# Optimization experiments

Measured on AMD Instinct MI355X. Metric: run time of the kernel, lower is better.

## Reference

```python
import jax, jax.numpy as jnp
import numpy as np

BETA = 0.9
THRESHOLD = 1.0
ATAN_ALPHA = 2.0  # snntorch ATan surrogate default


def setup_inputs() -> dict:
    key = jax.random.key(0)
    k1, k2 = jax.random.split(key)
    T, B, NI, NO = 100, 128, 2048, 1024
    x = jax.random.normal(k1, (T, B, NI), dtype=jnp.float32)
    # Kaiming-uniform-ish init like nn.Linear
    bound = 1.0 / np.sqrt(NI)
    W = jax.random.uniform(k2, (NO, NI), dtype=jnp.float32, minval=-bound, maxval=bound)
    return {"x": x, "W": W}


def _heaviside(u):
    return (u > 0).astype(u.dtype)


def reference(x, W):
    # cur[t] = x[t] @ W.T for all timesteps at once: [T, B, NO]
    cur = jnp.einsum('tbi,oi->tbo', x, W)

    def step(mem, cur_t):
        # snntorch Leaky (reset_mechanism='subtract'):
        #   reset = heaviside(mem_prev - threshold)   (detached)
        #   mem   = beta * mem_prev + cur - reset * threshold
        #   spk   = heaviside(mem - threshold)
        reset = _heaviside(mem - THRESHOLD)
        mem_new = BETA * mem + cur_t - reset * THRESHOLD
        spk = _heaviside(mem_new - THRESHOLD)
        return mem_new, (spk, mem_new)

    mem0 = jnp.zeros(cur.shape[1:], dtype=cur.dtype)  # [B, NO]
    _, (spk_rec, mem_rec) = jax.lax.scan(step, mem0, cur)
    return spk_rec, mem_rec
```

## Files before the change

### kernel.cpp

```cpp
#include <hip/hip_runtime.h>

#define T_STEPS 100
#define BATCH   128
#define NI      2048
#define NO      1024
#define M_TOT   (T_STEPS * BATCH)
#define TOTAL   (T_STEPS * BATCH * NO)
#define BNTOT   (BATCH * NO)
#define X_ELEMS (M_TOT * NI)

#define BMf 128
#define BNf 128
#define BKf 32
#define LDT 132
#define NXB (NO / BNf)
#define NYB (M_TOT/BMf)

__global__ __launch_bounds__(256, 2) void gemm_chain512(const float* __restrict__ X,
                                                        const float* __restrict__ W,
                                                        float* __restrict__ p0,
                                                        float* __restrict__ p1,
                                                        float* __restrict__ p2,
                                                        float* __restrict__ p3) {
    __shared__ float As[BKf][LDT];
    __shared__ float Bs[BKf][LDT];

    const int orig  = blockIdx.x;
    const int xcd   = orig & 7;
    const int q     = orig >> 3;
    const int n0    = (q & 7) * BNf;
    const int s     = q >> 3;
    const int p     = xcd * 50 + s;
    const int chain = p / 100;
    const int m0    = (p - chain * 100) * BMf;
    const int kbase = chain * 512;
    float* out = (chain == 0) ? p0 : (chain == 1) ? p1 : (chain == 2) ? p2 : p3;

    const int tid = threadIdx.x;
    const int tx  = tid & 15;
    const int ty  = tid >> 4;

    const int sr = tid >> 1;
    const int sk = (tid & 1) * 16;

    float ch[8][8] = {};

    #pragma unroll 1
    for (int k0 = kbase; k0 < kbase + 512; k0 += BKf) {
        #pragma unroll
        for (int qq = 0; qq < 4; ++qq) {
            const int kb = sk + qq * 4;
            const float4 fa = *reinterpret_cast<const float4*>(
                &X[(size_t)(m0 + sr) * NI + k0 + kb]);
            As[kb + 0][sr] = fa.x; As[kb + 1][sr] = fa.y;
            As[kb + 2][sr] = fa.z; As[kb + 3][sr] = fa.w;
            const float4 fb = *reinterpret_cast<const float4*>(
                &W[(size_t)(n0 + sr) * NI + k0 + kb]);
            Bs[kb + 0][sr] = fb.x; Bs[kb + 1][sr] = fb.y;
            Bs[kb + 2][sr] = fb.z; Bs[kb + 3][sr] = fb.w;
        }
        __syncthreads();

        #pragma unroll
        for (int kk = 0; kk < BKf; ++kk) {
            float a[8], b[8];
            *reinterpret_cast<float4*>(&a[0]) =
                *reinterpret_cast<const float4*>(&As[kk][ty * 4]);
            *reinterpret_cast<float4*>(&a[4]) =
                *reinterpret_cast<const float4*>(&As[kk][64 + ty * 4]);
            *reinterpret_cast<float4*>(&b[0]) =
                *reinterpret_cast<const float4*>(&Bs[kk][tx * 4]);
            *reinterpret_cast<float4*>(&b[4]) =
                *reinterpret_cast<const float4*>(&Bs[kk][64 + tx * 4]);
            #pragma unroll
            for (int i = 0; i < 8; ++i)
                #pragma unroll
                for (int j = 0; j < 8; ++j)
                    ch[i][j] = __fmaf_rn(a[i], b[j], ch[i][j]);
        }
        __syncthreads();
    }

    #pragma unroll
    for (int i = 0; i < 8; ++i) {
        const int row = m0 + ((i < 4) ? (ty * 4 + i) : (64 + ty * 4 + i - 4));
        const size_t rowbase = (size_t)row * NO + n0;
        #pragma unroll
        for (int h = 0; h < 2; ++h) {
            float4 v;
            v.x = ch[i][h * 4 + 0]; v.y = ch[i][h * 4 + 1];
            v.z = ch[i][h * 4 + 2]; v.w = ch[i][h * 4 + 3];
            *reinterpret_cast<float4*>(&out[rowbase + h * 64 + tx * 4]) = v;
        }
    }
}

__global__ __launch_bounds__(256) void fold_scan(float* __restrict__ spk,
                                                 float* __restrict__ memf,
                                                 const float* __restrict__ p2,
                                                 const float* __restrict__ p3) {
    const int idx = (blockIdx.x * blockDim.x + threadIdx.x) * 4;
    float4 mem = make_float4(0.f, 0.f, 0.f, 0.f);
    for (int t = 0; t < T_STEPS; ++t) {
        const size_t i = (size_t)t * BNTOT + idx;
        const float4 c0 = *reinterpret_cast<const float4*>(&spk[i]);
        const float4 c1 = *reinterpret_cast<const float4*>(&memf[i]);
        const float4 c2 = *reinterpret_cast<const float4*>(&p2[i]);
        const float4 c3 = *reinterpret_cast<const float4*>(&p3[i]);
        float4 spkv;
        #define STEP(c)                                                     \
        {                                                                   \
            const float cur = __fadd_rn(__fadd_rn(__fadd_rn(c0.c, c1.c),    \
                                                  c2.c), c3.c);             \
            const float reset = (mem.c > 1.0f) ? 1.0f : 0.0f;               \
            float tmp = __fmul_rn(0.9f, mem.c);                             \
            tmp = __fadd_rn(tmp, cur);                                      \
            mem.c = __fsub_rn(tmp, reset);                                  \
            spkv.c = (mem.c > 1.0f) ? 1.0f : 0.0f;                          \
        }
        STEP(x) STEP(y) STEP(z) STEP(w)
        #undef STEP
        *reinterpret_cast<float4*>(&spk[i])  = spkv;
        *reinterpret_cast<float4*>(&memf[i]) = mem;
    }
}

#define BMs 64
#define LDAs (BMs + 4)
#define NYBs (M_TOT / BMs)
#define YPXs (NYBs / 8)

__global__ __launch_bounds__(256) void gemm_512fold(const float* __restrict__ X,
                                                    const float* __restrict__ W,
                                                    float* __restrict__ curOut) {
    __shared__ float As[BKf][LDAs];
    __shared__ float Bs[BKf][LDT];
    const int orig = blockIdx.x;
    const int k_x  = orig & 7;
    const int q    = orig >> 3;
    const int m0   = (k_x * YPXs + (q >> 3)) * BMs;
    const int n0   = (q & 7) * BNf;
    const int tid = threadIdx.x;
    const int tx  = tid & 15;
    const int ty  = tid >> 4;
    const int ar = tid >> 2;
    const int ak = (tid & 3) * 4;
    const int br = tid >> 1;
    const int bk = (tid & 1) * 4;
    float ch[4][8]  = {};
    float tot[4][8] = {};
    #pragma unroll 1
    for (int k0 = 0; k0 < NI; k0 += BKf) {
        if (k0 == 512 || k0 == 1024 || k0 == 1536) {
            #pragma unroll
            for (int i = 0; i < 4; ++i)
                #pragma unroll
                for (int j = 0; j < 8; ++j) {
                    tot[i][j] = __fadd_rn(tot[i][j], ch[i][j]);
                    ch[i][j]  = 0.0f;
                }
        }
        {
            const float4 fa0 = *reinterpret_cast<const float4*>(
                &X[(size_t)(m0 + ar) * NI + k0 + ak]);
            const float4 fa1 = *reinterpret_cast<const float4*>(
                &X[(size_t)(m0 + ar) * NI + k0 + ak + 16]);
            As[ak + 0][ar] = fa0.x;  As[ak + 1][ar] = fa0.y;
            As[ak + 2][ar] = fa0.z;  As[ak + 3][ar] = fa0.w;
            As[ak + 16][ar] = fa1.x; As[ak + 17][ar] = fa1.y;
            As[ak + 18][ar] = fa1.z; As[ak + 19][ar] = fa1.w;
            #pragma unroll
            for (int qq = 0; qq < 4; ++qq) {
                const int kb = bk + qq * 8;
                const float4 fb = *reinterpret_cast<const float4*>(
                    &W[(size_t)(n0 + br) * NI + k0 + kb]);
                Bs[kb + 0][br] = fb.x; Bs[kb + 1][br] = fb.y;
                Bs[kb + 2][br] = fb.z; Bs[kb + 3][br] = fb.w;
            }
        }
        __syncthreads();
        #pragma unroll
        for (int kk = 0; kk < BKf; ++kk) {
            float a[4], b[8];
            *reinterpret_cast<float4*>(&a[0]) =
                *reinterpret_cast<const float4*>(&As[kk][ty * 4]);
            *reinterpret_cast<float4*>(&b[0]) =
                *reinterpret_cast<const float4*>(&Bs[kk][tx * 4]);
            *reinterpret_cast<float4*>(&b[4]) =
                *reinterpret_cast<const float4*>(&Bs[kk][64 + tx * 4]);
            #pragma unroll
            for (int i = 0; i < 4; ++i)
                #pragma unroll
                for (int j = 0; j < 8; ++j)
                    ch[i][j] = __fmaf_rn(a[i], b[j], ch[i][j]);
        }
        __syncthreads();
    }
    #pragma unroll
    for (int i = 0; i < 4; ++i) {
        const size_t rowbase = (size_t)(m0 + ty * 4 + i) * NO + n0;
        #pragma unroll
        for (int h = 0; h < 2; ++h) {
            float4 v;
            v.x = __fadd_rn(tot[i][h * 4 + 0], ch[i][h * 4 + 0]);
            v.y = __fadd_rn(tot[i][h * 4 + 1], ch[i][h * 4 + 1]);
            v.z = __fadd_rn(tot[i][h * 4 + 2], ch[i][h * 4 + 2]);
            v.w = __fadd_rn(tot[i][h * 4 + 3], ch[i][h * 4 + 3]);
            *reinterpret_cast<float4*>(&curOut[rowbase + h * 64 + tx * 4]) = v;
        }
    }
}

__global__ __launch_bounds__(256) void lif_scan(float* __restrict__ spk,
                                                float* __restrict__ memf) {
    const int idx = (blockIdx.x * blockDim.x + threadIdx.x) * 4;
    float4 mem = make_float4(0.f, 0.f, 0.f, 0.f);
    for (int t = 0; t < T_STEPS; ++t) {
        const size_t i = (size_t)t * BNTOT + idx;
        const float4 cur = *reinterpret_cast<const float4*>(&memf[i]);
        float4 spkv;
        #define STEP(c)                                                   \
        {                                                                 \
            const float reset = (mem.c > 1.0f) ? 1.0f : 0.0f;             \
            float tmp = __fmul_rn(0.9f, mem.c);                           \
            tmp = __fadd_rn(tmp, cur.c);                                  \
            mem.c = __fsub_rn(tmp, reset);                                \
            spkv.c = (mem.c > 1.0f) ? 1.0f : 0.0f;                        \
        }
        STEP(x) STEP(y) STEP(z) STEP(w)
        #undef STEP
        *reinterpret_cast<float4*>(&spk[i])  = spkv;
        *reinterpret_cast<float4*>(&memf[i]) = mem;
    }
}

extern "C" void kernel_launch(void* const* d_in, const int* in_sizes, int n_in,
                              void* d_out, int out_size, void* d_ws, size_t ws_size,
                              hipStream_t stream) {
    const float* X;
    const float* W;
    if (in_sizes[0] == X_ELEMS) { X = (const float*)d_in[0]; W = (const float*)d_in[1]; }
    else                        { X = (const float*)d_in[1]; W = (const float*)d_in[0]; }

    float* spk  = (float*)d_out;
    float* memf = spk + TOTAL;

    if (ws_size >= (size_t)2 * TOTAL * sizeof(float)) {
        float* p2 = (float*)d_ws;
        float* p3 = p2 + TOTAL;
        gemm_chain512<<<4 * NXB * NYB, 256, 0, stream>>>(X, W, spk, memf, p2, p3);
        fold_scan<<<BNTOT / 4 / 256, 256, 0, stream>>>(spk, memf, p2, p3);
    } else {
        gemm_512fold<<<NXB * NYBs, 256, 0, stream>>>(X, W, memf);
        lif_scan<<<BNTOT / 4 / 256, 256, 0, stream>>>(spk, memf);
    }
}
```

Measured before the change: 635.5 us.

## Load GEMM tiles directly to LDS with XOR-swizzled row-major layout

The chain GEMM kernel now uses the global_load_lds builtin to copy 16-byte chunks of X and W straight into shared memory. This bypasses the register staging and transposed scalar LDS stores. The tiles are kept row-major along K with an XOR swizzle to avoid bank conflicts, and each thread reads float4 slices along K and computes a strided 8x8 output. The trade-offs are that the 2-blocks-per-SM launch bound is dropped and the output stores become scalar and strided instead of float4. The other GEMM kernel only gets renamed constants.

```diff
diff --git a/kernel.cpp b/kernel.cpp
--- a/kernel.cpp
+++ b/kernel.cpp
@@ -12,86 +12,90 @@
 #define BMf 128
 #define BNf 128
 #define BKf 32
-#define LDT 132
+#define KSL 8
 #define NXB (NO / BNf)
 #define NYB (M_TOT/BMf)
 
-__global__ __launch_bounds__(256, 2) void gemm_chain512(const float* __restrict__ X,
-                                                        const float* __restrict__ W,
-                                                        float* __restrict__ p0,
-                                                        float* __restrict__ p1,
-                                                        float* __restrict__ p2,
-                                                        float* __restrict__ p3) {
-    __shared__ float As[BKf][LDT];
-    __shared__ float Bs[BKf][LDT];
+__device__ __forceinline__ void glds16(const float* g, float* l) {
+    __builtin_amdgcn_global_load_lds(
+        (const __attribute__((address_space(1))) void*)g,
+        (__attribute__((address_space(3))) void*)l, 16, 0, 0);
+}
+
+__global__ __launch_bounds__(256) void gemm_chain512(const float* __restrict__ X,
+                                                     const float* __restrict__ W,
+                                                     float* __restrict__ p0,
+                                                     float* __restrict__ p1,
+                                                     float* __restrict__ p2,
+                                                     float* __restrict__ p3) {
+    __shared__ float As[BMf][32];
+    __shared__ float Bs[BNf][32];
 
     const int orig  = blockIdx.x;
     const int xcd   = orig & 7;
     const int q     = orig >> 3;
     const int n0    = (q & 7) * BNf;
-    const int s     = q >> 3;
-    const int p     = xcd * 50 + s;
-    const int chain = p / 100;
-    const int m0    = (p - chain * 100) * BMf;
+    const int sq    = q >> 3;
+    const int pp    = xcd * 50 + sq;
+    const int chain = pp / 100;
+    const int m0    = (pp - chain * 100) * BMf;
     const int kbase = chain * 512;
     float* out = (chain == 0) ? p0 : (chain == 1) ? p1 : (chain == 2) ? p2 : p3;
 
     const int tid = threadIdx.x;
     const int tx  = tid & 15;
     const int ty  = tid >> 4;
-
-    const int sr = tid >> 1;
-    const int sk = (tid & 1) * 16;
-
-    float ch[8][8] = {};
+    const int w   = tid >> 6;
+    const int l   = tid & 63;
+    const int lr  = l >> 3;
+    const int swz = (l & 7) ^ lr;
+
+    const float* pA = X + (size_t)(m0 + w * 32 + lr) * NI + kbase + swz * 4;
+    const float* pB = W + (size_t)(n0 + w * 32 + lr) * NI + kbase + swz * 4;
+
+    const int ty7 = ty & 7;
+    const int tx7 = tx & 7;
+
+    float acc[8][8] = {};
 
     #pragma unroll 1
-    for (int k0 = kbase; k0 < kbase + 512; k0 += BKf) {
-        #pragma unroll
-        for (int qq = 0; qq < 4; ++qq) {
-            const int kb = sk + qq * 4;
-            const float4 fa = *reinterpret_cast<const float4*>(
-                &X[(size_t)(m0 + sr) * NI + k0 + kb]);
-            As[kb + 0][sr] = fa.x; As[kb + 1][sr] = fa.y;
-            As[kb + 2][sr] = fa.z; As[kb + 3][sr] = fa.w;
-            const float4 fb = *reinterpret_cast<const float4*>(
-                &W[(size_t)(n0 + sr) * NI + k0 + kb]);
-            Bs[kb + 0][sr] = fb.x; Bs[kb + 1][sr] = fb.y;
-            Bs[kb + 2][sr] = fb.z; Bs[kb + 3][sr] = fb.w;
-        }
-        __syncthreads();
-
-        #pragma unroll
-        for (int kk = 0; kk < BKf; ++kk) {
-            float a[8], b[8];
-            *reinterpret_cast<float4*>(&a[0]) =
-                *reinterpret_cast<const float4*>(&As[kk][ty * 4]);
-            *reinterpret_cast<float4*>(&a[4]) =
-                *reinterpret_cast<const float4*>(&As[kk][64 + ty * 4]);
-            *reinterpret_cast<float4*>(&b[0]) =
-                *reinterpret_cast<const float4*>(&Bs[kk][tx * 4]);
-            *reinterpret_cast<float4*>(&b[4]) =
-                *reinterpret_cast<const float4*>(&Bs[kk][64 + tx * 4]);
+    for (int k0 = 0; k0 < 512; k0 += BKf) {
+        #pragma unroll
+        for (int c = 0; c < 4; ++c) {
+            glds16(pA + k0 + (size_t)c * 8 * NI, &As[w * 32 + c * 8][0]);
+            glds16(pB + k0 + (size_t)c * 8 * NI, &Bs[w * 32 + c * 8][0]);
+        }
+        __syncthreads();
+
+        #pragma unroll
+        for (int ss = 0; ss < KSL; ++ss) {
+            const int oA = (ss ^ ty7) << 2;
+            const int oB = (ss ^ tx7) << 2;
+            float4 a4[8];
             #pragma unroll
             for (int i = 0; i < 8; ++i)
+                a4[i] = *reinterpret_cast<const float4*>(&As[ty + 16 * i][oA]);
+            #pragma unroll
+            for (int j = 0; j < 8; ++j) {
+                const float4 b4 = *reinterpret_cast<const float4*>(&Bs[tx + 16 * j][oB]);
                 #pragma unroll
-                for (int j = 0; j < 8; ++j)
-                    ch[i][j] = __fmaf_rn(a[i], b[j], ch[i][j]);
+                for (int i = 0; i < 8; ++i) {
+                    acc[i][j] = __fmaf_rn(a4[i].x, b4.x, acc[i][j]);
+                    acc[i][j] = __fmaf_rn(a4[i].y, b4.y, acc[i][j]);
+                    acc[i][j] = __fmaf_rn(a4[i].z, b4.z, acc[i][j]);
+                    acc[i][j] = __fmaf_rn(a4[i].w, b4.w, acc[i][j]);
+                }
+            }
         }
         __syncthreads();
     }
 
     #pragma unroll
     for (int i = 0; i < 8; ++i) {
-        const int row = m0 + ((i < 4) ? (ty * 4 + i) : (64 + ty * 4 + i - 4));
-        const size_t rowbase = (size_t)row * NO + n0;
-        #pragma unroll
-        for (int h = 0; h < 2; ++h) {
-            float4 v;
-            v.x = ch[i][h * 4 + 0]; v.y = ch[i][h * 4 + 1];
-            v.z = ch[i][h * 4 + 2]; v.w = ch[i][h * 4 + 3];
-            *reinterpret_cast<float4*>(&out[rowbase + h * 64 + tx * 4]) = v;
-        }
+        const size_t rowbase = (size_t)(m0 + ty + 16 * i) * NO + n0;
+        #pragma unroll
+        for (int j = 0; j < 8; ++j)
+            out[rowbase + tx + 16 * j] = acc[i][j];
     }
 }
 
@@ -126,15 +130,17 @@
 }
 
 #define BMs 64
+#define BKs2 32
 #define LDAs (BMs + 4)
+#define LDBs (BNf + 4)
 #define NYBs (M_TOT / BMs)
 #define YPXs (NYBs / 8)
 
 __global__ __launch_bounds__(256) void gemm_512fold(const float* __restrict__ X,
                                                     const float* __restrict__ W,
                                                     float* __restrict__ curOut) {
-    __shared__ float As[BKf][LDAs];
-    __shared__ float Bs[BKf][LDT];
+    __shared__ float As[BKs2][LDAs];
+    __shared__ float Bs[BKs2][LDBs];
     const int orig = blockIdx.x;
     const int k_x  = orig & 7;
     const int q    = orig >> 3;
@@ -150,7 +156,7 @@
     float ch[4][8]  = {};
     float tot[4][8] = {};
     #pragma unroll 1
-    for (int k0 = 0; k0 < NI; k0 += BKf) {
+    for (int k0 = 0; k0 < NI; k0 += BKs2) {
         if (k0 == 512 || k0 == 1024 || k0 == 1536) {
             #pragma unroll
             for (int i = 0; i < 4; ++i)
@@ -180,7 +186,7 @@
         }
         __syncthreads();
         #pragma unroll
-        for (int kk = 0; kk < BKf; ++kk) {
+        for (int kk = 0; kk < BKs2; ++kk) {
             float a[4], b[8];
             *reinterpret_cast<float4*>(&a[0]) =
                 *reinterpret_cast<const float4*>(&As[kk][ty * 4]);
```

Measured after the change: 685.9 us. 7.9% more time.
